# Optimization experiments

Measured on AMD Instinct MI355X. Metric: run time of the kernel, lower is better.

Reference implementation:

```python
import jax, jax.numpy as jnp
import numpy as np

SIGMA = 1.0
KSIZE = 5
WEAK = 75.0
STRONG = 255.0
LOW_T = 0.00392
HIGH_T = 0.15

# scipy.signal.gaussian(M, std): unnormalized gaussian window
_n = np.arange(KSIZE, dtype=np.float32) - (KSIZE - 1) / 2.0
_g = np.exp(-0.5 * (_n / SIGMA) ** 2).astype(np.float32)
GAUSS_H = jnp.asarray(_g.reshape(1, 1, 1, KSIZE))  # horizontal 1xK
GAUSS_V = jnp.asarray(_g.reshape(1, 1, KSIZE, 1))  # vertical Kx1

_sobel = np.array([[1, 0, -1], [2, 0, -2], [1, 0, -1]], dtype=np.float32)
SOBEL_H = jnp.asarray(_sobel.reshape(1, 1, 3, 3))
SOBEL_V = jnp.asarray(_sobel.T.reshape(1, 1, 3, 3))

_f0 = np.array([[0, 0, 0], [0, 1, -1], [0, 0, 0]], np.float32)
_f45 = np.array([[0, 0, 0], [0, 1, 0], [0, 0, -1]], np.float32)
_f90 = np.array([[0, 0, 0], [0, 1, 0], [0, -1, 0]], np.float32)
_f135 = np.array([[0, 0, 0], [0, 1, 0], [-1, 0, 0]], np.float32)
_f180 = np.array([[0, 0, 0], [-1, 1, 0], [0, 0, 0]], np.float32)
_f225 = np.array([[-1, 0, 0], [0, 1, 0], [0, 0, 0]], np.float32)
_f270 = np.array([[0, -1, 0], [0, 1, 0], [0, 0, 0]], np.float32)
_f315 = np.array([[0, 0, -1], [0, 1, 0], [0, 0, 0]], np.float32)
DIR_FILT = jnp.asarray(np.stack([_f0, _f45, _f90, _f135, _f180, _f225, _f270, _f315]).reshape(8, 1, 3, 3))

NBR_FILT = jnp.asarray(np.array([[1, 1, 1], [1, 0, 1], [1, 1, 1]], np.float32).reshape(1, 1, 3, 3))


def _conv(x, w, pad):
    # cross-correlation, matching torch F.conv2d
    return jax.lax.conv_general_dilated(
        x, w, window_strides=(1, 1), padding=[(pad[0], pad[0]), (pad[1], pad[1])],
        dimension_numbers=('NCHW', 'OIHW', 'NCHW'))


def setup_inputs() -> dict:
    key = jax.random.key(0)
    img = jax.random.uniform(key, (16, 1, 1024, 1024), dtype=jnp.float32)
    return {"img": img}


def reference(img):
    B = img.shape[0]
    # --- gaussian noise removal (separable) ---
    sm = _conv(img, GAUSS_H, (0, KSIZE // 2))
    sm = _conv(sm, GAUSS_V, (KSIZE // 2, 0))
    # --- sobel gradients ---
    Ix = _conv(sm, SOBEL_H, (1, 1))
    Iy = _conv(sm, SOBEL_V, (1, 1))
    mag = jnp.sqrt(Ix ** 2 + Iy ** 2)
    mag = mag / mag.reshape(B, -1).max(axis=1).reshape(B, 1, 1, 1)
    direction = jnp.arctan2(Iy, Ix) * (180.0 / 3.1415926) + 180.0
    direction = jnp.round(direction / 45.0) * 45.0
    # --- non-max suppression via directional differences + gather ---
    all_filtered = _conv(mag, DIR_FILT, (1, 1))  # [B,8,H,W]
    idx_pos = (direction / 45.0).astype(jnp.int32) % 8  # [B,1,H,W]
    idx_neg = (idx_pos + 4) % 8
    cs_pos = jnp.take_along_axis(all_filtered, idx_pos, axis=1)
    cs_neg = jnp.take_along_axis(all_filtered, idx_neg, axis=1)
    is_max = jnp.minimum(cs_pos, cs_neg) > 0.0
    thin = jnp.where(is_max, mag, 0.0)
    # --- double threshold ---
    hi = thin.max() * HIGH_T  # global max, as in source
    strong = thin >= hi
    weak = (thin < hi) & (thin >= LOW_T)
    inter = jnp.where(strong, STRONG, jnp.where(weak, WEAK, 0.0))
    # --- hysteresis: iterate until no weak pixel gains a strong neighbor ---
    def cond(state):
        return state[1]

    def body(state):
        x, _ = state
        weak_m = x == WEAK
        sn = _conv((x == STRONG).astype(jnp.float32), NBR_FILT, (1, 1))
        new_strong = weak_m & (sn > 0.0)
        x = jnp.where(new_strong, STRONG, x)
        return x, new_strong.any()

    final, _ = jax.lax.while_loop(cond, body, (inter, jnp.asarray(True)))
    final = jnp.where(final == STRONG, final, 0.0)
    return final
```

## Files before the change

kernel.cpp:

```cpp
#include <hip/hip_runtime.h>
#include <math.h>

#define BB 16
#define H 1024
#define W 1024
#define HW (H*W)
#define NTOT (BB*HW)

typedef unsigned long long u64;

__device__ __constant__ float GW[5] = {
    0.13533528323661270f, 0.60653065971263342f, 1.0f,
    0.60653065971263342f, 0.13533528323661270f};

__device__ __constant__ int NBDY[8] = {0, 1, 1, 1, 0, -1, -1, -1};
__device__ __constant__ int NBDX[8] = {1, 1, 0, -1, -1, -1, 0, 1};

#define CSCALE ((float)(180.0 / 3.1415926))

__device__ __forceinline__ float atan_poly01(float xin) {
    float y0 = 0.0f, x = xin;
    if (xin > 0.41421356f) {
        x = __fdividef(xin - 1.0f, xin + 1.0f);
        y0 = 0.78539816339f;
    }
    float z = x * x;
    float p = ((8.05374449538e-2f * z - 1.38776856032e-1f) * z + 1.99777106478e-1f) * z
              - 3.33329491539e-1f;
    return y0 + (p * z * x + x);
}

#define TW 128
#define TH 16
__global__ __launch_bounds__(256, 6) void k_smooth_sobel(const float* __restrict__ img,
                                                         float* __restrict__ mag,
                                                         unsigned char* __restrict__ bucket,
                                                         float* __restrict__ partial) {
#pragma clang fp contract(off)
    __shared__ float sA[22 * 136 + 16];
    __shared__ float sB[22 * 132];
    __shared__ float red[256];

    const int tid = threadIdx.x;
    const int x0 = blockIdx.x * TW;
    const int y0 = blockIdx.y * TH;
    const int b = blockIdx.z;
    const size_t base = (size_t)b * HW;

    for (int idx = tid; idx < 22 * 34; idx += 256) {
        int r = idx / 34, v = idx - r * 34;
        int gy = y0 - 3 + r;
        int gxv = x0 - 4 + v * 4;
        float4 val = make_float4(0.f, 0.f, 0.f, 0.f);
        if (gy >= 0 && gy < H && gxv >= 0 && gxv <= W - 4)
            val = *(const float4*)&img[base + (size_t)gy * W + gxv];
        *(float4*)&sA[r * 136 + v * 4] = val;
    }
    __syncthreads();

    for (int idx = tid; idx < 22 * 33; idx += 256) {
        int r = idx / 33, g = idx - r * 33;
        const float* p = &sA[r * 136 + g * 4];
        float4 A0 = *(const float4*)p;
        float4 A1 = *(const float4*)(p + 4);
        float4 A2 = *(const float4*)(p + 8);
        float a_[12] = {A0.x, A0.y, A0.z, A0.w, A1.x, A1.y, A1.z, A1.w,
                        A2.x, A2.y, A2.z, A2.w};
        float o[4];
#pragma unroll
        for (int j = 0; j < 4; ++j) {
            float s = 0.0f;
#pragma unroll
            for (int k = 0; k < 5; ++k) s = s + GW[k] * a_[j + 1 + k];
            o[j] = s;
        }
        *(float4*)&sB[r * 132 + g * 4] = make_float4(o[0], o[1], o[2], o[3]);
    }
    __syncthreads();

    for (int idx = tid; idx < 18 * 33; idx += 256) {
        int rr = idx / 33, g = idx - rr * 33;
        float bb[20];
#pragma unroll
        for (int k = 0; k < 5; ++k) {
            float4 t = *(const float4*)&sB[(rr + k) * 132 + g * 4];
            bb[k * 4 + 0] = t.x; bb[k * 4 + 1] = t.y;
            bb[k * 4 + 2] = t.z; bb[k * 4 + 3] = t.w;
        }
        int gy = y0 - 1 + rr;
        bool rowok = (gy >= 0 && gy < H);
        float o[4];
#pragma unroll
        for (int j = 0; j < 4; ++j) {
            float s = 0.0f;
#pragma unroll
            for (int k = 0; k < 5; ++k) s = s + GW[k] * bb[k * 4 + j];
            int gx = x0 - 1 + g * 4 + j;
            o[j] = (rowok && gx >= 0 && gx < W) ? s : 0.0f;
        }
        *(float4*)&sA[rr * 136 + g * 4] = make_float4(o[0], o[1], o[2], o[3]);
    }
    __syncthreads();

    float tmax = 0.0f;
#pragma unroll
    for (int k2 = 0; k2 < 2; ++k2) {
        int v = tid + k2 * 256;
        int r = v >> 5;
        int cg = (v & 31) * 4;
        int y = y0 + r;
        const float* P0 = &sA[r * 136 + cg];
        const float* P1 = P0 + 136;
        const float* P2 = P1 + 136;
        float4 q0 = *(const float4*)P0; float2 e0 = *(const float2*)(P0 + 4);
        float4 q1 = *(const float4*)P1; float2 e1 = *(const float2*)(P1 + 4);
        float4 q2 = *(const float4*)P2; float2 e2 = *(const float2*)(P2 + 4);
        float r0[6] = {q0.x, q0.y, q0.z, q0.w, e0.x, e0.y};
        float r1[6] = {q1.x, q1.y, q1.z, q1.w, e1.x, e1.y};
        float r2[6] = {q2.x, q2.y, q2.z, q2.w, e2.x, e2.y};

        float mg[4];
        unsigned int bk = 0;
#pragma unroll
        for (int j = 0; j < 4; ++j) {
            float a00 = r0[j], a01 = r0[j + 1], a02 = r0[j + 2];
            float a10 = r1[j],                  a12 = r1[j + 2];
            float a20 = r2[j], a21 = r2[j + 1], a22 = r2[j + 2];

            float Ix = a00;
            Ix = Ix - a02;
            Ix = Ix + 2.0f * a10;
            Ix = Ix - 2.0f * a12;
            Ix = Ix + a20;
            Ix = Ix - a22;

            float Iy = a00;
            Iy = Iy + 2.0f * a01;
            Iy = Iy + a02;
            Iy = Iy - a20;
            Iy = Iy - 2.0f * a21;
            Iy = Iy - a22;

            float t1 = Ix * Ix;
            float t2 = Iy * Iy;
            float m = sqrtf(t1 + t2);
            mg[j] = m;
            tmax = fmaxf(tmax, m);

            float ax = fabsf(Ix), ay = fabsf(Iy);
            float mn = fminf(ax, ay), mx = fmaxf(ax, ay);
            float zr = __fdividef(mn, mx);
            float bse = atan_poly01(zr);
            float phi = (ay > ax) ? (1.57079632679f - bse) : bse;
            if (Ix < 0.0f) phi = 3.14159265359f - phi;
            float theta = (Iy >= 0.0f) ? phi : -phi;
            float t = (theta * CSCALE + 180.0f) * (1.0f / 45.0f);
            float rr2 = rintf(t);
            if ((mx < 1e-30f) || (0.5f - fabsf(t - rr2) < 1e-4f)) {
                float fa2 = (float)atan2((double)Iy, (double)Ix);
                float d2 = fa2 * CSCALE;
                d2 = d2 + 180.0f;
                float t2d = d2 / 45.0f;
                rr2 = rintf(t2d);
            }
            int bidx = ((int)rr2) & 7;
            bk |= ((unsigned int)bidx) << (8 * j);
        }
        *(float4*)&mag[base + (size_t)y * W + x0 + cg] = make_float4(mg[0], mg[1], mg[2], mg[3]);
        *(unsigned int*)&bucket[base + (size_t)y * W + x0 + cg] = bk;
    }

    red[tid] = tmax;
    __syncthreads();
    for (int s = 128; s > 0; s >>= 1) {
        if (tid < s) red[tid] = fmaxf(red[tid], red[tid + s]);
        __syncthreads();
    }
    if (tid == 0) {
        int pb = (blockIdx.z * 64 + blockIdx.y) * 8 + blockIdx.x;
        partial[pb] = red[0];
    }
}

__global__ __launch_bounds__(256) void k_redmax_img(const float* __restrict__ partial,
                                                    float* __restrict__ magmax) {
    __shared__ float red[256];
    const float* p = partial + blockIdx.x * 512;
    float m = fmaxf(p[threadIdx.x], p[threadIdx.x + 256]);
    red[threadIdx.x] = m;
    __syncthreads();
    for (int s = 128; s > 0; s >>= 1) {
        if (threadIdx.x < s) red[threadIdx.x] = fmaxf(red[threadIdx.x], red[threadIdx.x + s]);
        __syncthreads();
    }
    if (threadIdx.x == 0) magmax[blockIdx.x] = red[0];
}

__global__ __launch_bounds__(1024) void k_redmax_all(const float* __restrict__ partial,
                                                     float* __restrict__ thinmax) {
    __shared__ float red[1024];
    float m = 0.0f;
    for (int k = threadIdx.x; k < 4096; k += 1024) m = fmaxf(m, partial[k]);
    red[threadIdx.x] = m;
    __syncthreads();
    for (int s = 512; s > 0; s >>= 1) {
        if (threadIdx.x < s) red[threadIdx.x] = fmaxf(red[threadIdx.x], red[threadIdx.x + s]);
        __syncthreads();
    }
    if (threadIdx.x == 0) *thinmax = red[0];
}

__global__ __launch_bounds__(256, 8) void k_nms_b(const float* __restrict__ mag,
                                                  const unsigned char* __restrict__ bucket,
                                                  const float* __restrict__ magmax,
                                                  u64* __restrict__ Mb,
                                                  float* __restrict__ partial) {
#pragma clang fp contract(off)
    __shared__ float sN[34 * 136];
    __shared__ float red[256];

    const int tid = threadIdx.x;
    const int x0 = blockIdx.x * 128;
    const int y0 = blockIdx.y * 32;
    const int b = blockIdx.z;
    const size_t base = (size_t)b * HW;
    const float M = magmax[b];

    for (int idx = tid; idx < 34 * 34; idx += 256) {
        int r = idx / 34, v = idx - r * 34;
        int gy = y0 - 1 + r;
        int gxv = x0 - 4 + v * 4;
        float4 val = make_float4(0.f, 0.f, 0.f, 0.f);
        if (gy >= 0 && gy < H && gxv >= 0 && gxv <= W - 4)
            val = *(const float4*)&mag[base + (size_t)gy * W + gxv];
        *(float4*)&sN[r * 136 + v * 4] = val;
    }
    __syncthreads();

    const int wv = tid >> 6, L = tid & 63;
    const int h = wv & 1, wr = wv >> 1;
    const int txw = (x0 >> 6) + h;
    float amax = 0.0f;

#pragma unroll
    for (int i = 0; i < 16; ++i) {
        int r = i * 2 + wr;
        int c = h * 64 + L;
        int y = y0 + r;
        unsigned int bkt = bucket[base + (size_t)y * W + x0 + c];
        int dy = NBDY[bkt], dx = NBDX[bkt];
        float a  = sN[(r + 1) * 136 + c + 4];
        float bp = sN[(r + 1 + dy) * 136 + c + 4 + dx];
        float bn = sN[(r + 1 - dy) * 136 + c + 4 - dx];
        bool g1 = a > bp, g2 = a > bn;
        bool f1 = a >= bp * 1.0000005f;
        bool f2 = a >= bn * 1.0000005f;
        bool r1 = g1, r2 = g2;
        if (__any((g1 && !f1) || (g2 && !f2))) {
            float qa = a / M;
            if (g1 && !f1) r1 = qa > (bp / M);
            if (g2 && !f2) r2 = qa > (bn / M);
        }
        bool im = r1 && r2;
        if (im) amax = fmaxf(amax, a);
        u64 word = __ballot(im);
        if (L == 0) {
            int ty = y >> 6, row = y & 63;
            Mb[((b << 8) | (ty << 4) | txw) * 64 + row] = word;
        }
    }

    red[tid] = amax;
    __syncthreads();
    for (int s = 128; s > 0; s >>= 1) {
        if (tid < s) red[tid] = fmaxf(red[tid], red[tid + s]);
        __syncthreads();
    }
    if (tid == 0)
        partial[(blockIdx.z * 32 + blockIdx.y) * 8 + blockIdx.x] = red[0] / M;
}

__global__ void k_bisect(const float* __restrict__ hdr, float* __restrict__ thr) {
    int t = threadIdx.x;
    if (t >= 32) return;
    int b = t >> 1;
    float M = hdr[b];
    float T = (t & 1) ? (hdr[16] * 0.15f) : 0.00392f;
    if (0.0f / M >= T) { thr[t] = 0.0f; return; }
    unsigned int lo = 0u, hi = 0x7f800000u;
    while (hi - lo > 1u) {
        unsigned int mid = lo + ((hi - lo) >> 1);
        if (__uint_as_float(mid) / M >= T) hi = mid; else lo = mid;
    }
    thr[t] = __uint_as_float(hi);
}

__global__ __launch_bounds__(256) void k_thresh_b(const float* __restrict__ mag,
                                                  const u64* __restrict__ Mb,
                                                  const float* __restrict__ hdr,
                                                  const float* __restrict__ thr,
                                                  u64* __restrict__ Sb,
                                                  u64* __restrict__ Wb) {
    const int tid = threadIdx.x;
    const int x0 = blockIdx.x * 128;
    const int y0 = blockIdx.y * 32;
    const int b = blockIdx.z;
    const size_t base = (size_t)b * HW;
    const float Alo = thr[b * 2], Ahi = thr[b * 2 + 1];
    const bool snm = (hdr[16] * 0.15f <= 0.0f);
    const int wv = tid >> 6, L = tid & 63;
    const int h = wv & 1, wr = wv >> 1;
    const int txw = (x0 >> 6) + h;

#pragma unroll
    for (int i = 0; i < 16; ++i) {
        int r = i * 2 + wr;
        int y = y0 + r;
        float a = mag[base + (size_t)y * W + x0 + h * 64 + L];
        int ty = y >> 6, row = y & 63;
        int widx = ((b << 8) | (ty << 4) | txw) * 64 + row;
        bool im = (Mb[widx] >> L) & 1ull;
        bool strong = snm || (im && (a >= Ahi));
        bool weak = (!strong) && im && (a >= Alo);
        u64 sw = __ballot(strong);
        u64 ww = __ballot(weak);
        if (L == 0) { Sb[widx] = sw; Wb[widx] = ww; }
    }
}

__global__ __launch_bounds__(256) void k_hyster_bits(const u64* __restrict__ Wb,
                                                     u64* __restrict__ Sb) {
    const int lane = threadIdx.x & 63;
    const int t = blockIdx.x * 4 + (threadIdx.x >> 6);
    const int ty = (t >> 4) & 15;
    const int tx = t & 15;
    const int idx = t * 64 + lane;

    u64 S = Sb[idx];
    const u64 Wk = Wb[idx];

    u64 hstat = 0;
    if (tx > 0)  hstat |= (Sb[(t - 1) * 64 + lane] >> 63) & 1ull;
    if (tx < 15) hstat |= (Sb[(t + 1) * 64 + lane] & 1ull) << 63;

    u64 halo = 0;
    if (lane == 0 && ty > 0) {
        const int ta = t - 16;
        u64 tc = Sb[ta * 64 + 63];
        u64 hh = (tc << 1) | tc | (tc >> 1);
        if (tx > 0)  hh |= (Sb[(ta - 1) * 64 + 63] >> 63) & 1ull;
        if (tx < 15) hh |= (Sb[(ta + 1) * 64 + 63] & 1ull) << 63;
        halo = hh;
    }
    if (lane == 63 && ty < 15) {
        const int tb = t + 16;
        u64 tc = Sb[tb * 64 + 0];
        u64 hh = (tc << 1) | tc | (tc >> 1);
        if (tx > 0)  hh |= (Sb[(tb - 1) * 64 + 0] >> 63) & 1ull;
        if (tx < 15) hh |= (Sb[(tb + 1) * 64 + 0] & 1ull) << 63;
        halo = hh;
    }

    for (int it = 0; it < 160; ++it) {
        u64 hh = (S << 1) | S | (S >> 1) | hstat;
        u64 up = __shfl_up(hh, 1, 64);
        if (lane == 0) up = halo;
        u64 dn = __shfl_down(hh, 1, 64);
        if (lane == 63) dn = halo;
        u64 dil = hh | up | dn;
        u64 nS = S | (Wk & dil);
        bool ch = (nS != S);
        S = nS;
        if (!__any(ch)) break;
    }

    Sb[idx] = S;
}

__global__ __launch_bounds__(256) void k_final4(const u64* __restrict__ Sb,
                                                float* __restrict__ out) {
    const int gid = blockIdx.x * 256 + threadIdx.x;
    const int p0 = gid * 4;
    const int x = p0 & (W - 1);
    const int y = (p0 >> 10) & (H - 1);
    const int b = p0 >> 20;
    const int widx = ((b << 8) | ((y >> 6) << 4) | (x >> 6)) * 64 + (y & 63);
    const u64 w = Sb[widx];
    const unsigned int nib = (unsigned int)((w >> (x & 63)) & 0xFull);
    float4 o;
    o.x = (nib & 1u) ? 255.0f : 0.0f;
    o.y = (nib & 2u) ? 255.0f : 0.0f;
    o.z = (nib & 4u) ? 255.0f : 0.0f;
    o.w = (nib & 8u) ? 255.0f : 0.0f;
    *(float4*)&out[p0] = o;
}

extern "C" void kernel_launch(void* const* d_in, const int* in_sizes, int n_in,
                              void* d_out, int out_size, void* d_ws, size_t ws_size,
                              hipStream_t stream) {
    (void)in_sizes; (void)n_in; (void)out_size; (void)ws_size;
    const float* img = (const float*)d_in[0];
    float* out = (float*)d_out;

    float* hdr = (float*)d_ws;
    float* thr = hdr + 64;
    float* partialA = hdr + 128;
    float* partialB = partialA + 8192;
    float* A = partialB + 4096;
    unsigned char* C = (unsigned char*)(A + (size_t)NTOT);
    u64* Sb = (u64*)(C + (size_t)NTOT);
    u64* Wb = Sb + NTOT / 64;
    u64* Mb = Wb + NTOT / 64;

    dim3 blk(256);
    k_smooth_sobel<<<dim3(8, 64, BB), blk, 0, stream>>>(img, A, C, partialA);
    k_redmax_img<<<dim3(BB), blk, 0, stream>>>(partialA, hdr);
    k_nms_b<<<dim3(8, 32, BB), blk, 0, stream>>>(A, C, hdr, Mb, partialB);
    k_redmax_all<<<dim3(1), dim3(1024), 0, stream>>>(partialB, hdr + 16);
    k_bisect<<<dim3(1), dim3(64), 0, stream>>>(hdr, thr);
    k_thresh_b<<<dim3(8, 32, BB), blk, 0, stream>>>(A, Mb, hdr, thr, Sb, Wb);
    for (int p = 0; p < 6; ++p)
        k_hyster_bits<<<dim3(NTOT / (64 * 64) / 4), blk, 0, stream>>>(Wb, Sb);
    k_final4<<<dim3(NTOT / 1024), blk, 0, stream>>>(Sb, out);
}
```

Baseline: 268.1 us.

## Shrink sobel tiles, replace atan with sector tests, fuse reductions and final write

```diff
diff --git a/kernel.cpp b/kernel.cpp
--- a/kernel.cpp
+++ b/kernel.cpp
@@ -18,27 +18,15 @@
 
 #define CSCALE ((float)(180.0 / 3.1415926))
 
-__device__ __forceinline__ float atan_poly01(float xin) {
-    float y0 = 0.0f, x = xin;
-    if (xin > 0.41421356f) {
-        x = __fdividef(xin - 1.0f, xin + 1.0f);
-        y0 = 0.78539816339f;
-    }
-    float z = x * x;
-    float p = ((8.05374449538e-2f * z - 1.38776856032e-1f) * z + 1.99777106478e-1f) * z
-              - 3.33329491539e-1f;
-    return y0 + (p * z * x + x);
-}
-
 #define TW 128
-#define TH 16
-__global__ __launch_bounds__(256, 6) void k_smooth_sobel(const float* __restrict__ img,
+#define TH 8
+__global__ __launch_bounds__(256, 8) void k_smooth_sobel(const float* __restrict__ img,
                                                          float* __restrict__ mag,
                                                          unsigned char* __restrict__ bucket,
                                                          float* __restrict__ partial) {
 #pragma clang fp contract(off)
-    __shared__ float sA[22 * 136 + 16];
-    __shared__ float sB[22 * 132];
+    __shared__ float sA[14 * 136 + 16];
+    __shared__ float sB[14 * 132];
     __shared__ float red[256];
 
     const int tid = threadIdx.x;
@@ -47,7 +35,7 @@
     const int b = blockIdx.z;
     const size_t base = (size_t)b * HW;
 
-    for (int idx = tid; idx < 22 * 34; idx += 256) {
+    for (int idx = tid; idx < 14 * 34; idx += 256) {
         int r = idx / 34, v = idx - r * 34;
         int gy = y0 - 3 + r;
         int gxv = x0 - 4 + v * 4;
@@ -58,7 +46,7 @@
     }
     __syncthreads();
 
-    for (int idx = tid; idx < 22 * 33; idx += 256) {
+    for (int idx = tid; idx < 14 * 33; idx += 256) {
         int r = idx / 33, g = idx - r * 33;
         const float* p = &sA[r * 136 + g * 4];
         float4 A0 = *(const float4*)p;
@@ -78,7 +66,7 @@
     }
     __syncthreads();
 
-    for (int idx = tid; idx < 18 * 33; idx += 256) {
+    for (int idx = tid; idx < 10 * 33; idx += 256) {
         int rr = idx / 33, g = idx - rr * 33;
         float bb[20];
 #pragma unroll
@@ -102,73 +90,71 @@
     }
     __syncthreads();
 
+    const int r = tid >> 5;
+    const int cg = (tid & 31) * 4;
+    const int y = y0 + r;
+    const float* P0 = &sA[r * 136 + cg];
+    const float* P1 = P0 + 136;
+    const float* P2 = P1 + 136;
+    float4 q0 = *(const float4*)P0; float2 e0 = *(const float2*)(P0 + 4);
+    float4 q1 = *(const float4*)P1; float2 e1 = *(const float2*)(P1 + 4);
+    float4 q2 = *(const float4*)P2; float2 e2 = *(const float2*)(P2 + 4);
+    float r0[6] = {q0.x, q0.y, q0.z, q0.w, e0.x, e0.y};
+    float r1[6] = {q1.x, q1.y, q1.z, q1.w, e1.x, e1.y};
+    float r2[6] = {q2.x, q2.y, q2.z, q2.w, e2.x, e2.y};
+
     float tmax = 0.0f;
-#pragma unroll
-    for (int k2 = 0; k2 < 2; ++k2) {
-        int v = tid + k2 * 256;
-        int r = v >> 5;
-        int cg = (v & 31) * 4;
-        int y = y0 + r;
-        const float* P0 = &sA[r * 136 + cg];
-        const float* P1 = P0 + 136;
-        const float* P2 = P1 + 136;
-        float4 q0 = *(const float4*)P0; float2 e0 = *(const float2*)(P0 + 4);
-        float4 q1 = *(const float4*)P1; float2 e1 = *(const float2*)(P1 + 4);
-        float4 q2 = *(const float4*)P2; float2 e2 = *(const float2*)(P2 + 4);
-        float r0[6] = {q0.x, q0.y, q0.z, q0.w, e0.x, e0.y};
-        float r1[6] = {q1.x, q1.y, q1.z, q1.w, e1.x, e1.y};
-        float r2[6] = {q2.x, q2.y, q2.z, q2.w, e2.x, e2.y};
-
-        float mg[4];
-        unsigned int bk = 0;
-#pragma unroll
-        for (int j = 0; j < 4; ++j) {
-            float a00 = r0[j], a01 = r0[j + 1], a02 = r0[j + 2];
-            float a10 = r1[j],                  a12 = r1[j + 2];
-            float a20 = r2[j], a21 = r2[j + 1], a22 = r2[j + 2];
-
-            float Ix = a00;
-            Ix = Ix - a02;
-            Ix = Ix + 2.0f * a10;
-            Ix = Ix - 2.0f * a12;
-            Ix = Ix + a20;
-            Ix = Ix - a22;
-
-            float Iy = a00;
-            Iy = Iy + 2.0f * a01;
-            Iy = Iy + a02;
-            Iy = Iy - a20;
-            Iy = Iy - 2.0f * a21;
-            Iy = Iy - a22;
-
-            float t1 = Ix * Ix;
-            float t2 = Iy * Iy;
-            float m = sqrtf(t1 + t2);
-            mg[j] = m;
-            tmax = fmaxf(tmax, m);
-
-            float ax = fabsf(Ix), ay = fabsf(Iy);
-            float mn = fminf(ax, ay), mx = fmaxf(ax, ay);
-            float zr = __fdividef(mn, mx);
-            float bse = atan_poly01(zr);
-            float phi = (ay > ax) ? (1.57079632679f - bse) : bse;
-            if (Ix < 0.0f) phi = 3.14159265359f - phi;
-            float theta = (Iy >= 0.0f) ? phi : -phi;
-            float t = (theta * CSCALE + 180.0f) * (1.0f / 45.0f);
-            float rr2 = rintf(t);
-            if ((mx < 1e-30f) || (0.5f - fabsf(t - rr2) < 1e-4f)) {
-                float fa2 = (float)atan2((double)Iy, (double)Ix);
-                float d2 = fa2 * CSCALE;
-                d2 = d2 + 180.0f;
-                float t2d = d2 / 45.0f;
-                rr2 = rintf(t2d);
-            }
-            int bidx = ((int)rr2) & 7;
-            bk |= ((unsigned int)bidx) << (8 * j);
-        }
-        *(float4*)&mag[base + (size_t)y * W + x0 + cg] = make_float4(mg[0], mg[1], mg[2], mg[3]);
-        *(unsigned int*)&bucket[base + (size_t)y * W + x0 + cg] = bk;
-    }
+    float mg[4];
+    unsigned int bk = 0;
+#pragma unroll
+    for (int j = 0; j < 4; ++j) {
+        float a00 = r0[j], a01 = r0[j + 1], a02 = r0[j + 2];
+        float a10 = r1[j],                  a12 = r1[j + 2];
+        float a20 = r2[j], a21 = r2[j + 1], a22 = r2[j + 2];
+
+        float Ix = a00;
+        Ix = Ix - a02;
+        Ix = Ix + 2.0f * a10;
+        Ix = Ix - 2.0f * a12;
+        Ix = Ix + a20;
+        Ix = Ix - a22;
+
+        float Iy = a00;
+        Iy = Iy + 2.0f * a01;
+        Iy = Iy + a02;
+        Iy = Iy - a20;
+        Iy = Iy - 2.0f * a21;
+        Iy = Iy - a22;
+
+        float t1 = Ix * Ix;
+        float t2 = Iy * Iy;
+        float m = sqrtf(t1 + t2);
+        mg[j] = m;
+        tmax = fmaxf(tmax, m);
+
+        float ax = fabsf(Ix), ay = fabsf(Iy);
+        float mn = fminf(ax, ay), mx = fmaxf(ax, ay);
+        float cr = mn * 0.92387953f - mx * 0.38268343f;
+        int bidx;
+        if (fabsf(cr) < mx * 3e-5f) {
+            float fa2 = (float)atan2((double)Iy, (double)Ix);
+            float d2 = fa2 * CSCALE;
+            d2 = d2 + 180.0f;
+            float t2d = d2 / 45.0f;
+            float rr2 = rintf(t2d);
+            bidx = ((int)rr2) & 7;
+        } else if (ay <= ax * 0.41421356f) {
+            bidx = signbit(Ix) ? 0 : 4;
+        } else if (ay >= ax * 2.41421356f) {
+            bidx = (Iy >= 0.0f) ? 6 : 2;
+        } else {
+            bidx = (Iy >= 0.0f) ? ((Ix >= 0.0f) ? 5 : 7)
+                                : ((Ix >= 0.0f) ? 3 : 1);
+        }
+        bk |= ((unsigned int)bidx) << (8 * j);
+    }
+    *(float4*)&mag[base + (size_t)y * W + x0 + cg] = make_float4(mg[0], mg[1], mg[2], mg[3]);
+    *(unsigned int*)&bucket[base + (size_t)y * W + x0 + cg] = bk;
 
     red[tid] = tmax;
     __syncthreads();
@@ -177,7 +163,7 @@
         __syncthreads();
     }
     if (tid == 0) {
-        int pb = (blockIdx.z * 64 + blockIdx.y) * 8 + blockIdx.x;
+        int pb = (blockIdx.z * 128 + blockIdx.y) * 8 + blockIdx.x;
         partial[pb] = red[0];
     }
 }
@@ -185,8 +171,9 @@
 __global__ __launch_bounds__(256) void k_redmax_img(const float* __restrict__ partial,
                                                     float* __restrict__ magmax) {
     __shared__ float red[256];
-    const float* p = partial + blockIdx.x * 512;
-    float m = fmaxf(p[threadIdx.x], p[threadIdx.x + 256]);
+    const float* p = partial + blockIdx.x * 1024;
+    float m = 0.0f;
+    for (int k = threadIdx.x; k < 1024; k += 256) m = fmaxf(m, p[k]);
     red[threadIdx.x] = m;
     __syncthreads();
     for (int s = 128; s > 0; s >>= 1) {
@@ -196,27 +183,14 @@
     if (threadIdx.x == 0) magmax[blockIdx.x] = red[0];
 }
 
-__global__ __launch_bounds__(1024) void k_redmax_all(const float* __restrict__ partial,
-                                                     float* __restrict__ thinmax) {
-    __shared__ float red[1024];
-    float m = 0.0f;
-    for (int k = threadIdx.x; k < 4096; k += 1024) m = fmaxf(m, partial[k]);
-    red[threadIdx.x] = m;
-    __syncthreads();
-    for (int s = 512; s > 0; s >>= 1) {
-        if (threadIdx.x < s) red[threadIdx.x] = fmaxf(red[threadIdx.x], red[threadIdx.x + s]);
-        __syncthreads();
-    }
-    if (threadIdx.x == 0) *thinmax = red[0];
-}
-
-__global__ __launch_bounds__(256, 8) void k_nms_b(const float* __restrict__ mag,
+__global__ __launch_bounds__(256, 6) void k_nms_b(const float* __restrict__ mag,
                                                   const unsigned char* __restrict__ bucket,
                                                   const float* __restrict__ magmax,
                                                   u64* __restrict__ Mb,
                                                   float* __restrict__ partial) {
 #pragma clang fp contract(off)
     __shared__ float sN[34 * 136];
+    __shared__ unsigned int nib32[256];
     __shared__ float red[256];
 
     const int tid = threadIdx.x;
@@ -237,37 +211,68 @@
     }
     __syncthreads();
 
-    const int wv = tid >> 6, L = tid & 63;
-    const int h = wv & 1, wr = wv >> 1;
-    const int txw = (x0 >> 6) + h;
+    const int r = tid >> 5;
+    const int cg = (tid & 31) * 4;
     float amax = 0.0f;
 
-#pragma unroll
-    for (int i = 0; i < 16; ++i) {
-        int r = i * 2 + wr;
-        int c = h * 64 + L;
-        int y = y0 + r;
-        unsigned int bkt = bucket[base + (size_t)y * W + x0 + c];
-        int dy = NBDY[bkt], dx = NBDX[bkt];
-        float a  = sN[(r + 1) * 136 + c + 4];
-        float bp = sN[(r + 1 + dy) * 136 + c + 4 + dx];
-        float bn = sN[(r + 1 - dy) * 136 + c + 4 - dx];
-        bool g1 = a > bp, g2 = a > bn;
-        bool f1 = a >= bp * 1.0000005f;
-        bool f2 = a >= bn * 1.0000005f;
-        bool r1 = g1, r2 = g2;
-        if (__any((g1 && !f1) || (g2 && !f2))) {
-            float qa = a / M;
-            if (g1 && !f1) r1 = qa > (bp / M);
-            if (g2 && !f2) r2 = qa > (bn / M);
-        }
-        bool im = r1 && r2;
-        if (im) amax = fmaxf(amax, a);
-        u64 word = __ballot(im);
-        if (L == 0) {
-            int ty = y >> 6, row = y & 63;
-            Mb[((b << 8) | (ty << 4) | txw) * 64 + row] = word;
-        }
+    for (int k4 = 0; k4 < 4; ++k4) {
+        const int rr = k4 * 8 + r;
+        const int y = y0 + rr;
+        unsigned int bk4 = *(const unsigned int*)&bucket[base + (size_t)y * W + x0 + cg];
+        float4 a4 = *(const float4*)&sN[(rr + 1) * 136 + cg + 4];
+        float av[4] = {a4.x, a4.y, a4.z, a4.w};
+        bool im[4];
+        bool bad = false;
+        float bpv[4], bnv[4];
+        bool g1v[4], g2v[4], f1v[4], f2v[4];
+#pragma unroll
+        for (int j = 0; j < 4; ++j) {
+            int c = cg + j;
+            int bkt = (bk4 >> (8 * j)) & 0xff;
+            int dy = NBDY[bkt], dx = NBDX[bkt];
+            float a = av[j];
+            float bp = sN[(rr + 1 + dy) * 136 + c + 4 + dx];
+            float bn = sN[(rr + 1 - dy) * 136 + c + 4 - dx];
+            bpv[j] = bp; bnv[j] = bn;
+            bool g1 = a > bp, g2 = a > bn;
+            bool f1 = a >= bp * 1.0000005f;
+            bool f2 = a >= bn * 1.0000005f;
+            g1v[j] = g1; g2v[j] = g2; f1v[j] = f1; f2v[j] = f2;
+            im[j] = g1 && g2;
+            bad = bad || (g1 && !f1) || (g2 && !f2);
+        }
+        if (__any(bad)) {
+#pragma unroll
+            for (int j = 0; j < 4; ++j) {
+                bool b1 = g1v[j] && !f1v[j];
+                bool b2 = g2v[j] && !f2v[j];
+                if (b1 || b2) {
+                    float qa = av[j] / M;
+                    bool r1 = g1v[j], r2 = g2v[j];
+                    if (b1) r1 = qa > (bpv[j] / M);
+                    if (b2) r2 = qa > (bnv[j] / M);
+                    im[j] = r1 && r2;
+                }
+            }
+        }
+        unsigned int nib = 0;
+#pragma unroll
+        for (int j = 0; j < 4; ++j) {
+            if (im[j]) { nib |= 1u << j; amax = fmaxf(amax, av[j]); }
+        }
+        nib32[tid] = nib;
+        __syncthreads();
+        if (tid < 16) {
+            int rw = tid >> 1, h = tid & 1;
+            u64 w = 0;
+#pragma unroll
+            for (int j = 0; j < 16; ++j)
+                w |= (u64)nib32[rw * 32 + h * 16 + j] << (4 * j);
+            int yy = y0 + k4 * 8 + rw;
+            int widx = ((b << 8) | ((yy >> 6) << 4) | ((x0 >> 6) + h)) * 64 + (yy & 63);
+            Mb[widx] = w;
+        }
+        __syncthreads();
     }
 
     red[tid] = amax;
@@ -280,27 +285,41 @@
         partial[(blockIdx.z * 32 + blockIdx.y) * 8 + blockIdx.x] = red[0] / M;
 }
 
-__global__ void k_bisect(const float* __restrict__ hdr, float* __restrict__ thr) {
-    int t = threadIdx.x;
-    if (t >= 32) return;
-    int b = t >> 1;
-    float M = hdr[b];
-    float T = (t & 1) ? (hdr[16] * 0.15f) : 0.00392f;
-    if (0.0f / M >= T) { thr[t] = 0.0f; return; }
-    unsigned int lo = 0u, hi = 0x7f800000u;
-    while (hi - lo > 1u) {
-        unsigned int mid = lo + ((hi - lo) >> 1);
-        if (__uint_as_float(mid) / M >= T) hi = mid; else lo = mid;
-    }
-    thr[t] = __uint_as_float(hi);
-}
-
-__global__ __launch_bounds__(256) void k_thresh_b(const float* __restrict__ mag,
-                                                  const u64* __restrict__ Mb,
-                                                  const float* __restrict__ hdr,
-                                                  const float* __restrict__ thr,
-                                                  u64* __restrict__ Sb,
-                                                  u64* __restrict__ Wb) {
+__global__ __launch_bounds__(1024) void k_finalize_thr(const float* __restrict__ partial,
+                                                       float* __restrict__ hdr,
+                                                       float* __restrict__ thr) {
+    __shared__ float red[1024];
+    float m = 0.0f;
+    for (int k = threadIdx.x; k < 4096; k += 1024) m = fmaxf(m, partial[k]);
+    red[threadIdx.x] = m;
+    __syncthreads();
+    for (int s = 512; s > 0; s >>= 1) {
+        if (threadIdx.x < s) red[threadIdx.x] = fmaxf(red[threadIdx.x], red[threadIdx.x + s]);
+        __syncthreads();
+    }
+    if (threadIdx.x == 0) hdr[16] = red[0];
+    if (threadIdx.x < 32) {
+        float tm = red[0];
+        int t = threadIdx.x;
+        float M = hdr[t >> 1];
+        float T = (t & 1) ? (tm * 0.15f) : 0.00392f;
+        if (0.0f / M >= T) { thr[t] = 0.0f; return; }
+        unsigned int lo = 0u, hi = 0x7f800000u;
+        while (hi - lo > 1u) {
+            unsigned int mid = lo + ((hi - lo) >> 1);
+            if (__uint_as_float(mid) / M >= T) hi = mid; else lo = mid;
+        }
+        thr[t] = __uint_as_float(hi);
+    }
+}
+
+__global__ __launch_bounds__(256, 8) void k_thresh_b(const float* __restrict__ mag,
+                                                     const u64* __restrict__ Mb,
+                                                     const float* __restrict__ hdr,
+                                                     const float* __restrict__ thr,
+                                                     u64* __restrict__ Sb,
+                                                     u64* __restrict__ Wb) {
+    __shared__ unsigned int nibS[256], nibW[256];
     const int tid = threadIdx.x;
     const int x0 = blockIdx.x * 128;
     const int y0 = blockIdx.y * 32;
@@ -308,28 +327,50 @@
     const size_t base = (size_t)b * HW;
     const float Alo = thr[b * 2], Ahi = thr[b * 2 + 1];
     const bool snm = (hdr[16] * 0.15f <= 0.0f);
-    const int wv = tid >> 6, L = tid & 63;
-    const int h = wv & 1, wr = wv >> 1;
-    const int txw = (x0 >> 6) + h;
-
-#pragma unroll
-    for (int i = 0; i < 16; ++i) {
-        int r = i * 2 + wr;
-        int y = y0 + r;
-        float a = mag[base + (size_t)y * W + x0 + h * 64 + L];
-        int ty = y >> 6, row = y & 63;
-        int widx = ((b << 8) | (ty << 4) | txw) * 64 + row;
-        bool im = (Mb[widx] >> L) & 1ull;
-        bool strong = snm || (im && (a >= Ahi));
-        bool weak = (!strong) && im && (a >= Alo);
-        u64 sw = __ballot(strong);
-        u64 ww = __ballot(weak);
-        if (L == 0) { Sb[widx] = sw; Wb[widx] = ww; }
-    }
-}
-
+    const int r = tid >> 5;
+    const int cg = (tid & 31) * 4;
+    const int hl = cg >> 6;
+
+    for (int k4 = 0; k4 < 4; ++k4) {
+        const int rr = k4 * 8 + r;
+        const int y = y0 + rr;
+        float4 a4 = *(const float4*)&mag[base + (size_t)y * W + x0 + cg];
+        float av[4] = {a4.x, a4.y, a4.z, a4.w};
+        const int widx = ((b << 8) | ((y >> 6) << 4) | ((x0 >> 6) + hl)) * 64 + (y & 63);
+        u64 mw = Mb[widx];
+        unsigned int ns = 0, nw = 0;
+#pragma unroll
+        for (int j = 0; j < 4; ++j) {
+            bool im = (mw >> ((cg & 63) + j)) & 1ull;
+            bool strong = snm || (im && (av[j] >= Ahi));
+            bool weak = (!strong) && im && (av[j] >= Alo);
+            ns |= (strong ? 1u : 0u) << j;
+            nw |= (weak ? 1u : 0u) << j;
+        }
+        nibS[tid] = ns;
+        nibW[tid] = nw;
+        __syncthreads();
+        if (tid < 32) {
+            bool isW = (tid >= 16);
+            int t = tid & 15;
+            int rw = t >> 1, h = t & 1;
+            const unsigned int* nb = isW ? nibW : nibS;
+            u64 w = 0;
+#pragma unroll
+            for (int j = 0; j < 16; ++j)
+                w |= (u64)nb[rw * 32 + h * 16 + j] << (4 * j);
+            int yy = y0 + k4 * 8 + rw;
+            int widx2 = ((b << 8) | ((yy >> 6) << 4) | ((x0 >> 6) + h)) * 64 + (yy & 63);
+            if (isW) Wb[widx2] = w; else Sb[widx2] = w;
+        }
+        __syncthreads();
+    }
+}
+
+template <bool LAST>
 __global__ __launch_bounds__(256) void k_hyster_bits(const u64* __restrict__ Wb,
-                                                     u64* __restrict__ Sb) {
+                                                     u64* __restrict__ Sb,
+                                                     float* __restrict__ out) {
     const int lane = threadIdx.x & 63;
     const int t = blockIdx.x * 4 + (threadIdx.x >> 6);
     const int ty = (t >> 4) & 15;
@@ -374,25 +415,17 @@
         if (!__any(ch)) break;
     }
 
-    Sb[idx] = S;
-}
-
-__global__ __launch_bounds__(256) void k_final4(const u64* __restrict__ Sb,
-                                                float* __restrict__ out) {
-    const int gid = blockIdx.x * 256 + threadIdx.x;
-    const int p0 = gid * 4;
-    const int x = p0 & (W - 1);
-    const int y = (p0 >> 10) & (H - 1);
-    const int b = p0 >> 20;
-    const int widx = ((b << 8) | ((y >> 6) << 4) | (x >> 6)) * 64 + (y & 63);
-    const u64 w = Sb[widx];
-    const unsigned int nib = (unsigned int)((w >> (x & 63)) & 0xFull);
-    float4 o;
-    o.x = (nib & 1u) ? 255.0f : 0.0f;
-    o.y = (nib & 2u) ? 255.0f : 0.0f;
-    o.z = (nib & 4u) ? 255.0f : 0.0f;
-    o.w = (nib & 8u) ? 255.0f : 0.0f;
-    *(float4*)&out[p0] = o;
+    if (!LAST) {
+        Sb[idx] = S;
+    } else {
+        const int bimg = t >> 8;
+        float* op = out + (size_t)bimg * HW + (size_t)(ty * 64) * W + tx * 64 + lane;
+#pragma unroll 4
+        for (int rr = 0; rr < 64; ++rr) {
+            u64 wrow = __shfl(S, rr, 64);
+            op[(size_t)rr * W] = ((wrow >> lane) & 1ull) ? 255.0f : 0.0f;
+        }
+    }
 }
 
 extern "C" void kernel_launch(void* const* d_in, const int* in_sizes, int n_in,
@@ -405,7 +438,7 @@
     float* hdr = (float*)d_ws;
     float* thr = hdr + 64;
     float* partialA = hdr + 128;
-    float* partialB = partialA + 8192;
+    float* partialB = partialA + 16384;
     float* A = partialB + 4096;
     unsigned char* C = (unsigned char*)(A + (size_t)NTOT);
     u64* Sb = (u64*)(C + (size_t)NTOT);
@@ -413,13 +446,12 @@
     u64* Mb = Wb + NTOT / 64;
 
     dim3 blk(256);
-    k_smooth_sobel<<<dim3(8, 64, BB), blk, 0, stream>>>(img, A, C, partialA);
+    k_smooth_sobel<<<dim3(8, 128, BB), blk, 0, stream>>>(img, A, C, partialA);
     k_redmax_img<<<dim3(BB), blk, 0, stream>>>(partialA, hdr);
     k_nms_b<<<dim3(8, 32, BB), blk, 0, stream>>>(A, C, hdr, Mb, partialB);
-    k_redmax_all<<<dim3(1), dim3(1024), 0, stream>>>(partialB, hdr + 16);
-    k_bisect<<<dim3(1), dim3(64), 0, stream>>>(hdr, thr);
+    k_finalize_thr<<<dim3(1), dim3(1024), 0, stream>>>(partialB, hdr, thr);
     k_thresh_b<<<dim3(8, 32, BB), blk, 0, stream>>>(A, Mb, hdr, thr, Sb, Wb);
-    for (int p = 0; p < 6; ++p)
-        k_hyster_bits<<<dim3(NTOT / (64 * 64) / 4), blk, 0, stream>>>(Wb, Sb);
-    k_final4<<<dim3(NTOT / 1024), blk, 0, stream>>>(Sb, out);
-}
+    for (int p = 0; p < 5; ++p)
+        k_hyster_bits<false><<<dim3(NTOT / (64 * 64) / 4), blk, 0, stream>>>(Wb, Sb, out);
+    k_hyster_bits<true><<<dim3(NTOT / (64 * 64) / 4), blk, 0, stream>>>(Wb, Sb, out);
+}
```

New measurement: 242.6 us. 9.5% less time.
